# Kernel tuning notes

Measured on AMD Instinct MI355X. Metric: run time of the kernel, lower is better.

The kernel has to match this reference:

```python
import jax, jax.numpy as jnp
import numpy as np

D_MODEL = 1024
NUM_HEADS = 16
HEAD_DIM = D_MODEL // NUM_HEADS


def setup_inputs() -> dict:
    key = jax.random.key(0)
    ks = jax.random.split(key, 12)
    B, S = 2, 2048
    scale = 1.0 / np.sqrt(D_MODEL)
    inp = {
        "x": jax.random.normal(ks[0], (B, S, D_MODEL), dtype=jnp.float32),
        "docking_scores": jax.random.uniform(ks[1], (B, S), dtype=jnp.float32),
        "q_w": jax.random.normal(ks[2], (D_MODEL, D_MODEL), dtype=jnp.float32) * scale,
        "q_b": jnp.zeros((D_MODEL,), dtype=jnp.float32),
        "k_w": jax.random.normal(ks[3], (D_MODEL, D_MODEL), dtype=jnp.float32) * scale,
        "k_b": jnp.zeros((D_MODEL,), dtype=jnp.float32),
        "v_w": jax.random.normal(ks[4], (D_MODEL, D_MODEL), dtype=jnp.float32) * scale,
        "v_b": jnp.zeros((D_MODEL,), dtype=jnp.float32),
        "o_w": jax.random.normal(ks[5], (D_MODEL, D_MODEL), dtype=jnp.float32) * scale,
        "o_b": jnp.zeros((D_MODEL,), dtype=jnp.float32),
        "alpha": jnp.float32(0.5),
    }
    return inp


def reference(x, docking_scores, q_w, q_b, k_w, k_b, v_w, v_b, o_w, o_b, alpha):
    B, S, _ = x.shape
    # Projections; weights stored as (in, out) so y = x @ W + b
    def proj(w, b):
        y = jnp.einsum('bsd,de->bse', x, w) + b
        return y.reshape(B, S, NUM_HEADS, HEAD_DIM).transpose(0, 2, 1, 3)  # (B,H,S,hd)
    Q = proj(q_w, q_b)
    K = proj(k_w, k_b)
    V = proj(v_w, v_b)
    scores = jnp.einsum('bhqd,bhkd->bhqk', Q, K) / np.sqrt(HEAD_DIM)
    attn = jax.nn.softmax(scores, axis=-1)  # (B,H,S,S)
    # post-softmax docking blend, broadcast over heads and query positions
    ds = docking_scores[:, None, None, :]  # (B,1,1,S)
    attn = (1.0 - alpha) * attn + alpha * ds
    ctx = jnp.einsum('bhqk,bhkd->bhqd', attn, V)
    ctx = ctx.transpose(0, 2, 1, 3).reshape(B, S, D_MODEL)
    return jnp.einsum('bsd,de->bse', ctx, o_w) + o_b
```

## Files before the change

kernel.cpp:

```cpp
#include <hip/hip_runtime.h>
#include <hip/hip_bf16.h>

typedef __attribute__((ext_vector_type(8)))  short bf16x8;
typedef __attribute__((ext_vector_type(4)))  float f32x4;
typedef __attribute__((ext_vector_type(16))) float f32x16;
typedef __attribute__((ext_vector_type(4)))  int   i32x4;
typedef __attribute__((ext_vector_type(4)))  unsigned short u16x4;
typedef __attribute__((ext_vector_type(8)))  unsigned short u16x8;

__device__ __forceinline__ unsigned short f2bf(float f) {
    unsigned int u = __builtin_bit_cast(unsigned int, f);
    u += 0x7FFFu + ((u >> 16) & 1u);
    return (unsigned short)(u >> 16);
}
__device__ __forceinline__ float bf2f(unsigned short h) {
    unsigned int u = ((unsigned int)h) << 16;
    return __builtin_bit_cast(float, u);
}
__device__ __forceinline__ bf16x8 ld16(const unsigned short* p) {
    return *reinterpret_cast<const bf16x8*>(p);
}
__device__ __forceinline__ float fexp2(float x) {
    float r; asm("v_exp_f32 %0, %1" : "=v"(r) : "v"(x)); return r;
}
__device__ __forceinline__ float frcp(float x) {
    float r; asm("v_rcp_f32 %0, %1" : "=v"(r) : "v"(x)); return r;
}
__device__ __forceinline__ void pswap(unsigned int& a, unsigned int& b) {
    asm("v_permlane32_swap_b32 %0, %1" : "+v"(a), "+v"(b));
}

__global__ void cvt_x_kernel(const float* __restrict__ in, unsigned short* __restrict__ out, int n8) {
    int idx = blockIdx.x * blockDim.x + threadIdx.x;
    int stride = gridDim.x * blockDim.x;
    for (int i = idx; i < n8; i += stride) {
        f32x4 a = reinterpret_cast<const f32x4*>(in)[i*2];
        f32x4 b = reinterpret_cast<const f32x4*>(in)[i*2+1];
        u16x8 o;
        o[0]=f2bf(a[0]); o[1]=f2bf(a[1]); o[2]=f2bf(a[2]); o[3]=f2bf(a[3]);
        o[4]=f2bf(b[0]); o[5]=f2bf(b[1]); o[6]=f2bf(b[2]); o[7]=f2bf(b[3]);
        reinterpret_cast<u16x8*>(out)[i] = o;
    }
}

__global__ void tr_w_kernel(const float* __restrict__ q_w, const float* __restrict__ k_w,
                            const float* __restrict__ v_w, const float* __restrict__ o_w,
                            unsigned short* __restrict__ WT) {
    __shared__ float tile[32][33];
    const float* W = (blockIdx.z == 0) ? q_w : (blockIdx.z == 1) ? k_w : (blockIdx.z == 2) ? v_w : o_w;
    unsigned short* dst = WT + (size_t)blockIdx.z * 1024 * 1024;
    int tx = threadIdx.x, ty = threadIdx.y;
    int n0 = blockIdx.x * 32, k0 = blockIdx.y * 32;
#pragma unroll
    for (int j = 0; j < 4; ++j)
        tile[ty + j*8][tx] = W[(size_t)(k0 + ty + j*8) * 1024 + n0 + tx];
    __syncthreads();
#pragma unroll
    for (int j = 0; j < 4; ++j)
        dst[(size_t)(n0 + ty + j*8) * 1024 + k0 + tx] = f2bf(tile[tx][ty + j*8]);
}

__global__ __launch_bounds__(256) void gemm_qkv(
    const unsigned short* __restrict__ A,
    const unsigned short* __restrict__ WT,
    const float* __restrict__ qb, const float* __restrict__ kbias, const float* __restrict__ vbias,
    unsigned short* __restrict__ Qo, unsigned short* __restrict__ Ko, unsigned short* __restrict__ Vto)
{
    __shared__ __align__(16) unsigned short As[128*64];
    __shared__ __align__(16) unsigned short Bs[128*64];
    const int tid = threadIdx.x, lane = tid & 63, w = tid >> 6;
    const int wm = w >> 1, wn = w & 1;
    const int m0 = blockIdx.y * 128, n0 = blockIdx.x * 128;
    const int K = 1024;
    f32x4 acc[4][4] = {};
    for (int k0 = 0; k0 < K; k0 += 64) {
#pragma unroll
        for (int j = 0; j < 4; ++j) {
            const int c = j*256 + tid, r = c >> 3, s = c & 7;
            __builtin_amdgcn_global_load_lds(
                (const __attribute__((address_space(1))) void*)&A[(size_t)(m0+r)*K + k0 + s*8],
                (__attribute__((address_space(3))) void*)&As[(size_t)c*8], 16, 0, 0);
            __builtin_amdgcn_global_load_lds(
                (const __attribute__((address_space(1))) void*)&WT[(size_t)(n0+r)*K + k0 + s*8],
                (__attribute__((address_space(3))) void*)&Bs[(size_t)c*8], 16, 0, 0);
        }
        __syncthreads();
#pragma unroll
        for (int kc = 0; kc < 2; ++kc) {
            bf16x8 af[4], bfr[4];
            const int slog = kc*4 + (lane >> 4);
#pragma unroll
            for (int t = 0; t < 4; ++t) {
                const int row = wm*64 + t*16 + (lane & 15);
                af[t]  = ld16(&As[row*64 + slog*8]);
                const int col = wn*64 + t*16 + (lane & 15);
                bfr[t] = ld16(&Bs[col*64 + slog*8]);
            }
#pragma unroll
            for (int mt = 0; mt < 4; ++mt)
#pragma unroll
                for (int nt = 0; nt < 4; ++nt)
                    acc[mt][nt] = __builtin_amdgcn_mfma_f32_16x16x32_bf16(af[mt], bfr[nt], acc[mt][nt], 0, 0, 0);
        }
        __syncthreads();
    }
    const int mat = n0 >> 10;
    if (mat == 2) {
#pragma unroll
        for (int mt = 0; mt < 4; ++mt)
#pragma unroll
        for (int nt = 0; nt < 4; ++nt) {
            const int nl = (n0 & 1023) + wn*64 + nt*16 + (lane & 15);
            const int h = nl >> 6, hd = nl & 63;
            const int mbase = m0 + wm*64 + mt*16 + ((lane >> 4) << 2);
            const int b = mbase >> 11, s = mbase & 2047;
            const float bv = vbias[nl];
            u16x4 pk;
#pragma unroll
            for (int r = 0; r < 4; ++r) pk[r] = f2bf(acc[mt][nt][r] + bv);
            *reinterpret_cast<u16x4*>(&Vto[((size_t)((b << 4) | h) * 64 + hd) * 2048 + s]) = pk;
        }
    } else {
        unsigned short* outp = mat ? Ko : Qo;
        const float* bias = mat ? kbias : qb;
        const float scale = mat ? 1.0f : 0.180336881f;
#pragma unroll
        for (int mt = 0; mt < 4; ++mt)
#pragma unroll
        for (int nt = 0; nt < 4; ++nt) {
            const int nl = (n0 & 1023) + wn*64 + nt*16 + (lane & 15);
            const int h = nl >> 6, hd = nl & 63;
            const int mbase = m0 + wm*64 + mt*16 + ((lane >> 4) << 2);
            const float bv = bias[nl];
#pragma unroll
            for (int r = 0; r < 4; ++r) {
                const int mm2 = mbase + r, b = mm2 >> 11, s = mm2 & 2047;
                outp[((size_t)((b << 4) | h) * 2048 + s) * 64 + hd] = f2bf((acc[mt][nt][r] + bv) * scale);
            }
        }
    }
}

__global__ __launch_bounds__(256) void gemm_o(
    const unsigned short* __restrict__ A, const unsigned short* __restrict__ WT,
    const float* __restrict__ bias, float* __restrict__ Cout)
{
    __shared__ __align__(16) unsigned short As[128*64];
    __shared__ __align__(16) unsigned short Bs[128*64];
    const int tid = threadIdx.x, lane = tid & 63, w = tid >> 6;
    const int wm = w >> 1, wn = w & 1;
    const int m0 = blockIdx.y * 128, n0 = blockIdx.x * 128;
    const int K = 1024;
    f32x4 acc[4][4] = {};
    for (int k0 = 0; k0 < K; k0 += 64) {
#pragma unroll
        for (int j = 0; j < 4; ++j) {
            const int c = j*256 + tid, r = c >> 3, s = c & 7;
            __builtin_amdgcn_global_load_lds(
                (const __attribute__((address_space(1))) void*)&A[(size_t)(m0+r)*K + k0 + s*8],
                (__attribute__((address_space(3))) void*)&As[(size_t)c*8], 16, 0, 0);
            __builtin_amdgcn_global_load_lds(
                (const __attribute__((address_space(1))) void*)&WT[(size_t)(n0+r)*K + k0 + s*8],
                (__attribute__((address_space(3))) void*)&Bs[(size_t)c*8], 16, 0, 0);
        }
        __syncthreads();
#pragma unroll
        for (int kc = 0; kc < 2; ++kc) {
            bf16x8 af[4], bfr[4];
            const int slog = kc*4 + (lane >> 4);
#pragma unroll
            for (int t = 0; t < 4; ++t) {
                const int row = wm*64 + t*16 + (lane & 15);
                af[t]  = ld16(&As[row*64 + slog*8]);
                const int col = wn*64 + t*16 + (lane & 15);
                bfr[t] = ld16(&Bs[col*64 + slog*8]);
            }
#pragma unroll
            for (int mt = 0; mt < 4; ++mt)
#pragma unroll
                for (int nt = 0; nt < 4; ++nt)
                    acc[mt][nt] = __builtin_amdgcn_mfma_f32_16x16x32_bf16(af[mt], bfr[nt], acc[mt][nt], 0, 0, 0);
        }
        __syncthreads();
    }
#pragma unroll
    for (int mt = 0; mt < 4; ++mt)
#pragma unroll
    for (int nt = 0; nt < 4; ++nt) {
        const int n = n0 + wn*64 + nt*16 + (lane & 15);
        const int mbase = m0 + wm*64 + mt*16 + ((lane >> 4) << 2);
        const float bv = bias[n];
#pragma unroll
        for (int r = 0; r < 4; ++r)
            Cout[(size_t)(mbase + r) * 1024 + n] = acc[mt][nt][r] + bv;
    }
}

__global__ void dock_c_kernel(const float* __restrict__ ds, const unsigned short* __restrict__ Vt,
                              float* __restrict__ cvec) {
    __shared__ float red[256];
    const int bh = blockIdx.x >> 3, sl = blockIdx.x & 7;
    const int b = bh >> 4;
    const int t = threadIdx.x, d = t & 63, q4 = t >> 6;
    const unsigned short* vrow = &Vt[(size_t)bh * 131072 + (size_t)d * 2048 + sl * 256 + q4 * 64];
    const float* dsr = &ds[b * 2048 + sl * 256 + q4 * 64];
    float sum = 0.f;
#pragma unroll
    for (int k = 0; k < 64; k += 8) {
        bf16x8 v = ld16(&vrow[k]);
#pragma unroll
        for (int i = 0; i < 8; ++i) sum += dsr[k + i] * bf2f((unsigned short)v[i]);
    }
    red[t] = sum;
    __syncthreads();
    if (t < 64) atomicAdd(&cvec[bh * 64 + t], red[t] + red[64 + t] + red[128 + t] + red[192 + t]);
}

__global__ __launch_bounds__(256, 2) void attn_kernel(
    const unsigned short* __restrict__ Qp,
    const unsigned short* __restrict__ Kp,
    const unsigned short* __restrict__ Vp,
    const float* __restrict__ cvec,
    const float* __restrict__ alpha_p,
    unsigned short* __restrict__ ctx)
{
    __shared__ __align__(16) unsigned short Ks[2][4096];
    __shared__ __align__(16) unsigned short Vs[2][4096];
    __shared__ float sml[4][32];
    const int tid = threadIdx.x, lane = tid & 63, w = tid >> 6;
    const int hi = lane >> 5, ln = lane & 31;
    const int wg = blockIdx.x;
    const int swz = (wg & 7) * 64 + (wg >> 3);
    const int bh = swz >> 4, qt = swz & 15;
    const int q0 = qt * 128 + w * 32;
    const size_t hb = (size_t)bh * (2048 * 64);
    const float alpha = *alpha_p;

    const int sr = tid >> 3, ss = tid & 7;
    const int ssw = (ss ^ (sr & 7)) << 3;
    const unsigned short* Kg = Kp + hb;
    const unsigned short* Vg = Vp + hb;

    bf16x8 qf[4];
    {
        const unsigned short* qr = &Qp[hb + (size_t)(q0 + ln) * 64 + hi * 8];
#pragma unroll
        for (int ks = 0; ks < 4; ++ks) qf[ks] = ld16(qr + ks * 16);
    }

    const short one_bf = (short)0x3F80;
    const bf16x8 onesf = {one_bf, one_bf, one_bf, one_bf, one_bf, one_bf, one_bf, one_bf};

    f32x16 oacc0 = {}, oacc1 = {}, lacc = {};
    float m = -1e30f;

    auto stage = [&](int buf, int it) {
#pragma unroll
        for (int p = 0; p < 2; ++p) {
            __builtin_amdgcn_global_load_lds(
                (const __attribute__((address_space(1))) void*)&Kg[(size_t)(it*64 + p*32 + sr) * 64 + ssw],
                (__attribute__((address_space(3))) void*)&Ks[buf][p*2048 + tid*8], 16, 0, 0);
            __builtin_amdgcn_global_load_lds(
                (const __attribute__((address_space(1))) void*)&Vg[(size_t)(p*32 + sr) * 2048 + it*64 + ssw],
                (__attribute__((address_space(3))) void*)&Vs[buf][p*2048 + tid*8], 16, 0, 0);
        }
    };

    bf16x8 kf[8];
    auto ldk = [&](const unsigned short* base) {
#pragma unroll
        for (int t2 = 0; t2 < 2; ++t2)
#pragma unroll
        for (int ks = 0; ks < 4; ++ks) {
            const int row = t2*32 + ln;
            const int sl  = ((ks*2 + hi) ^ (row & 7)) << 3;
            kf[t2*4+ks] = ld16(base + row*64 + sl);
        }
    };

    stage(0, 0);
    __syncthreads();
    stage(1, 1);
    ldk(&Ks[0][0]);
    f32x16 sA0 = {}, sA1 = {}, sB0 = {}, sB1 = {};
#pragma unroll
    for (int ks = 0; ks < 4; ++ks) {
        sA0 = __builtin_amdgcn_mfma_f32_32x32x16_bf16(kf[ks],   qf[ks], sA0, 0, 0, 0);
        sA1 = __builtin_amdgcn_mfma_f32_32x32x16_bf16(kf[4+ks], qf[ks], sA1, 0, 0, 0);
    }

    auto step = [&](f32x16& sc0, f32x16& sc1, f32x16& sn0, f32x16& sn1, int buf, int it) {
        bf16x8 vf[8];
#pragma unroll
        for (int t2 = 0; t2 < 2; ++t2)
#pragma unroll
        for (int ks = 0; ks < 4; ++ks) {
            const int row = t2*32 + ln;
            const int sl  = ((ks*2 + hi) ^ (row & 7)) << 3;
            vf[t2*4+ks] = ld16(&Vs[buf][row*64 + sl]);
        }
        __syncthreads();
        if (it + 2 < 32) stage(buf, it + 2);
        const bool more = (it + 1 < 32);
        if (more) ldk(&Ks[buf ^ 1][0]);
        __builtin_amdgcn_s_setprio(1);
        if (more) {
            sn0 = {}; sn1 = {};
#pragma unroll
            for (int ks = 0; ks < 4; ++ks) {
                sn0 = __builtin_amdgcn_mfma_f32_32x32x16_bf16(kf[ks],   qf[ks], sn0, 0, 0, 0);
                sn1 = __builtin_amdgcn_mfma_f32_32x32x16_bf16(kf[4+ks], qf[ks], sn1, 0, 0, 0);
            }
        }
        float mx[8];
#pragma unroll
        for (int r = 0; r < 8; ++r)
            mx[r] = fmaxf(fmaxf(sc0[r], sc0[r+8]), fmaxf(sc1[r], sc1[r+8]));
        float tm = fmaxf(fmaxf(fmaxf(mx[0],mx[1]), fmaxf(mx[2],mx[3])),
                         fmaxf(fmaxf(mx[4],mx[5]), fmaxf(mx[6],mx[7])));
        {
            unsigned int ua = __builtin_bit_cast(unsigned int, tm), ub = ua;
            pswap(ua, ub);
            tm = fmaxf(__builtin_bit_cast(float, ua), __builtin_bit_cast(float, ub));
        }
        if (__any(tm > m + 8.f)) {
            float mn = fmaxf(m, tm);
            float sc = fexp2(m - mn);
            m = mn;
            if (hi == 0) sml[w][ln] = sc;
#pragma unroll
            for (int m4 = 0; m4 < 4; ++m4) {
                f32x4 sv = *reinterpret_cast<const f32x4*>(&sml[w][m4*8 + hi*4]);
#pragma unroll
                for (int r3 = 0; r3 < 4; ++r3) {
                    oacc0[m4*4+r3] *= sv[r3];
                    oacc1[m4*4+r3] *= sv[r3];
                    lacc [m4*4+r3] *= sv[r3];
                }
            }
        }
        float p0a[16], p1a[16];
#pragma unroll
        for (int r = 0; r < 16; ++r) {
            p0a[r] = fexp2(sc0[r] - m);
            p1a[r] = fexp2(sc1[r] - m);
        }

        unsigned int Wp0[4][2], Wp1[4][2];
#pragma unroll
        for (int m4 = 0; m4 < 4; ++m4)
#pragma unroll
        for (int jj = 0; jj < 2; ++jj) {
            asm("v_cvt_pk_bf16_f32 %0, %1, %2" : "=v"(Wp0[m4][jj]) : "v"(p0a[m4*4+jj*2]), "v"(p0a[m4*4+jj*2+1]));
            asm("v_cvt_pk_bf16_f32 %0, %1, %2" : "=v"(Wp1[m4][jj]) : "v"(p1a[m4*4+jj*2]), "v"(p1a[m4*4+jj*2+1]));
        }
#pragma unroll
        for (int ks = 0; ks < 4; ++ks) {
            const int tp = ks & 1;
            unsigned int a0, a1, b0, b1;
            if (ks < 2) { a0 = Wp0[2*tp][0]; a1 = Wp0[2*tp][1]; b0 = Wp0[2*tp+1][0]; b1 = Wp0[2*tp+1][1]; }
            else        { a0 = Wp1[2*tp][0]; a1 = Wp1[2*tp][1]; b0 = Wp1[2*tp+1][0]; b1 = Wp1[2*tp+1][1]; }
            pswap(a0, b0);
            pswap(a1, b1);
            i32x4 pw;
            pw[0] = (int)a0; pw[1] = (int)a1; pw[2] = (int)b0; pw[3] = (int)b1;
            bf16x8 pf = __builtin_bit_cast(bf16x8, pw);
            oacc0 = __builtin_amdgcn_mfma_f32_32x32x16_bf16(pf, vf[ks],   oacc0, 0, 0, 0);
            oacc1 = __builtin_amdgcn_mfma_f32_32x32x16_bf16(pf, vf[4+ks], oacc1, 0, 0, 0);
            lacc  = __builtin_amdgcn_mfma_f32_32x32x16_bf16(pf, onesf,    lacc,  0, 0, 0);
        }
        __builtin_amdgcn_s_setprio(0);
    };

#pragma unroll 1
    for (int ii = 0; ii < 16; ++ii) {
        step(sA0, sA1, sB0, sB1, 0, ii*2);
        step(sB0, sB1, sA0, sA1, 1, ii*2 + 1);
    }

    const int b = bh >> 4, h = bh & 15;
    const float a1f = 1.f - alpha;
    const float cv0 = alpha * cvec[bh*64 + ln];
    const float cv1 = alpha * cvec[bh*64 + 32 + ln];
#pragma unroll
    for (int m4 = 0; m4 < 4; ++m4) {
#pragma unroll
        for (int r3 = 0; r3 < 4; ++r3) {
            const int row = m4*8 + hi*4 + r3;
            const int s = q0 + row;
            const float iv = frcp(lacc[m4*4 + r3]);
            unsigned short* orow = &ctx[((size_t)(b*2048 + s))*1024 + h*64 + ln];
            orow[0]  = f2bf(a1f * oacc0[m4*4+r3] * iv + cv0);
            orow[32] = f2bf(a1f * oacc1[m4*4+r3] * iv + cv1);
        }
    }
}

extern "C" void kernel_launch(void* const* d_in, const int* in_sizes, int n_in,
                              void* d_out, int out_size, void* d_ws, size_t ws_size,
                              hipStream_t stream) {
    const float* x     = (const float*)d_in[0];
    const float* ds    = (const float*)d_in[1];
    const float* q_w   = (const float*)d_in[2];
    const float* q_b   = (const float*)d_in[3];
    const float* k_w   = (const float*)d_in[4];
    const float* k_b   = (const float*)d_in[5];
    const float* v_w   = (const float*)d_in[6];
    const float* v_b   = (const float*)d_in[7];
    const float* o_w   = (const float*)d_in[8];
    const float* o_b   = (const float*)d_in[9];
    const float* alpha = (const float*)d_in[10];

    char* ws = (char*)d_ws;
    const size_t MB = 1024 * 1024;
    unsigned short* xb   = (unsigned short*)(ws);
    unsigned short* wT   = (unsigned short*)(ws + 8  * MB);
    unsigned short* Qb   = (unsigned short*)(ws + 16 * MB);
    unsigned short* Kb   = (unsigned short*)(ws + 24 * MB);
    unsigned short* Vt   = (unsigned short*)(ws + 32 * MB);
    float*          cvec = (float*)         (ws + 40 * MB);
    unsigned short* ctxb = xb;

    const int M = 4096, K = 1024;

    cvt_x_kernel<<<2048, 256, 0, stream>>>(x, xb, M * K / 8);

    dim3 tb(32, 8);
    dim3 tg(32, 32, 4);
    tr_w_kernel<<<tg, tb, 0, stream>>>(q_w, k_w, v_w, o_w, wT);

    dim3 gqkv(24, 32);
    gemm_qkv<<<gqkv, 256, 0, stream>>>(xb, wT, q_b, k_b, v_b, Qb, Kb, Vt);

    hipMemsetAsync(cvec, 0, 32 * 64 * sizeof(float), stream);
    dock_c_kernel<<<256, 256, 0, stream>>>(ds, Vt, cvec);

    attn_kernel<<<512, 256, 0, stream>>>(Qb, Kb, Vt, cvec, alpha, ctxb);

    dim3 go(8, 32);
    gemm_o<<<go, 256, 0, stream>>>(ctxb, wT + (size_t)3 * MB, o_b, (float*)d_out);
}
```

Baseline: 144.9 us.

## Double-buffer LDS and XOR-swizzle tiles in QKV and output projection GEMMs

Both projection GEMMs now use two LDS buffers, so the next K tile is prefetched with global_load_lds while MFMAs run on the current one, and one barrier per iteration is dropped. The source column chunk is XOR-swizzled by row so the later 16-byte LDS fragment reads avoid bank conflicts. LDS use per block doubles to 64KB, which may lower occupancy. The single barrier now guards both buffers, so the next stage is issued only after all waves have finished reading the previous buffer.

```diff
diff --git a/kernel.cpp b/kernel.cpp
--- a/kernel.cpp
+++ b/kernel.cpp
@@ -66,35 +66,46 @@
     const float* __restrict__ qb, const float* __restrict__ kbias, const float* __restrict__ vbias,
     unsigned short* __restrict__ Qo, unsigned short* __restrict__ Ko, unsigned short* __restrict__ Vto)
 {
-    __shared__ __align__(16) unsigned short As[128*64];
-    __shared__ __align__(16) unsigned short Bs[128*64];
+    __shared__ __align__(16) unsigned short As[2][128*64];
+    __shared__ __align__(16) unsigned short Bs[2][128*64];
     const int tid = threadIdx.x, lane = tid & 63, w = tid >> 6;
     const int wm = w >> 1, wn = w & 1;
     const int m0 = blockIdx.y * 128, n0 = blockIdx.x * 128;
     const int K = 1024;
+    const int sr = tid >> 3, ssl = tid & 7;
+    const int ssw = (ssl ^ (sr & 7)) << 3;
     f32x4 acc[4][4] = {};
-    for (int k0 = 0; k0 < K; k0 += 64) {
+
+    auto stage = [&](int buf, int k0) {
 #pragma unroll
         for (int j = 0; j < 4; ++j) {
-            const int c = j*256 + tid, r = c >> 3, s = c & 7;
-            __builtin_amdgcn_global_load_lds(
-                (const __attribute__((address_space(1))) void*)&A[(size_t)(m0+r)*K + k0 + s*8],
-                (__attribute__((address_space(3))) void*)&As[(size_t)c*8], 16, 0, 0);
-            __builtin_amdgcn_global_load_lds(
-                (const __attribute__((address_space(1))) void*)&WT[(size_t)(n0+r)*K + k0 + s*8],
-                (__attribute__((address_space(3))) void*)&Bs[(size_t)c*8], 16, 0, 0);
-        }
+            const int c = j*256 + tid, r = j*32 + sr;
+            __builtin_amdgcn_global_load_lds(
+                (const __attribute__((address_space(1))) void*)&A[(size_t)(m0+r)*K + k0 + ssw],
+                (__attribute__((address_space(3))) void*)&As[buf][(size_t)c*8], 16, 0, 0);
+            __builtin_amdgcn_global_load_lds(
+                (const __attribute__((address_space(1))) void*)&WT[(size_t)(n0+r)*K + k0 + ssw],
+                (__attribute__((address_space(3))) void*)&Bs[buf][(size_t)c*8], 16, 0, 0);
+        }
+    };
+
+    stage(0, 0);
+#pragma unroll 1
+    for (int t = 0; t < 16; ++t) {
         __syncthreads();
+        if (t < 15) stage((t + 1) & 1, (t + 1) * 64);
+        const unsigned short* pa = &As[t & 1][0];
+        const unsigned short* pb = &Bs[t & 1][0];
 #pragma unroll
         for (int kc = 0; kc < 2; ++kc) {
             bf16x8 af[4], bfr[4];
             const int slog = kc*4 + (lane >> 4);
 #pragma unroll
-            for (int t = 0; t < 4; ++t) {
-                const int row = wm*64 + t*16 + (lane & 15);
-                af[t]  = ld16(&As[row*64 + slog*8]);
-                const int col = wn*64 + t*16 + (lane & 15);
-                bfr[t] = ld16(&Bs[col*64 + slog*8]);
+            for (int t2 = 0; t2 < 4; ++t2) {
+                const int row = wm*64 + t2*16 + (lane & 15);
+                af[t2]  = ld16(&pa[row*64 + ((slog ^ (row & 7)) << 3)]);
+                const int col = wn*64 + t2*16 + (lane & 15);
+                bfr[t2] = ld16(&pb[col*64 + ((slog ^ (col & 7)) << 3)]);
             }
 #pragma unroll
             for (int mt = 0; mt < 4; ++mt)
@@ -102,7 +113,6 @@
                 for (int nt = 0; nt < 4; ++nt)
                     acc[mt][nt] = __builtin_amdgcn_mfma_f32_16x16x32_bf16(af[mt], bfr[nt], acc[mt][nt], 0, 0, 0);
         }
-        __syncthreads();
     }
     const int mat = n0 >> 10;
     if (mat == 2) {
@@ -145,35 +155,46 @@
     const unsigned short* __restrict__ A, const unsigned short* __restrict__ WT,
     const float* __restrict__ bias, float* __restrict__ Cout)
 {
-    __shared__ __align__(16) unsigned short As[128*64];
-    __shared__ __align__(16) unsigned short Bs[128*64];
+    __shared__ __align__(16) unsigned short As[2][128*64];
+    __shared__ __align__(16) unsigned short Bs[2][128*64];
     const int tid = threadIdx.x, lane = tid & 63, w = tid >> 6;
     const int wm = w >> 1, wn = w & 1;
     const int m0 = blockIdx.y * 128, n0 = blockIdx.x * 128;
     const int K = 1024;
+    const int sr = tid >> 3, ssl = tid & 7;
+    const int ssw = (ssl ^ (sr & 7)) << 3;
     f32x4 acc[4][4] = {};
-    for (int k0 = 0; k0 < K; k0 += 64) {
+
+    auto stage = [&](int buf, int k0) {
 #pragma unroll
         for (int j = 0; j < 4; ++j) {
-            const int c = j*256 + tid, r = c >> 3, s = c & 7;
-            __builtin_amdgcn_global_load_lds(
-                (const __attribute__((address_space(1))) void*)&A[(size_t)(m0+r)*K + k0 + s*8],
-                (__attribute__((address_space(3))) void*)&As[(size_t)c*8], 16, 0, 0);
-            __builtin_amdgcn_global_load_lds(
-                (const __attribute__((address_space(1))) void*)&WT[(size_t)(n0+r)*K + k0 + s*8],
-                (__attribute__((address_space(3))) void*)&Bs[(size_t)c*8], 16, 0, 0);
-        }
+            const int c = j*256 + tid, r = j*32 + sr;
+            __builtin_amdgcn_global_load_lds(
+                (const __attribute__((address_space(1))) void*)&A[(size_t)(m0+r)*K + k0 + ssw],
+                (__attribute__((address_space(3))) void*)&As[buf][(size_t)c*8], 16, 0, 0);
+            __builtin_amdgcn_global_load_lds(
+                (const __attribute__((address_space(1))) void*)&WT[(size_t)(n0+r)*K + k0 + ssw],
+                (__attribute__((address_space(3))) void*)&Bs[buf][(size_t)c*8], 16, 0, 0);
+        }
+    };
+
+    stage(0, 0);
+#pragma unroll 1
+    for (int t = 0; t < 16; ++t) {
         __syncthreads();
+        if (t < 15) stage((t + 1) & 1, (t + 1) * 64);
+        const unsigned short* pa = &As[t & 1][0];
+        const unsigned short* pb = &Bs[t & 1][0];
 #pragma unroll
         for (int kc = 0; kc < 2; ++kc) {
             bf16x8 af[4], bfr[4];
             const int slog = kc*4 + (lane >> 4);
 #pragma unroll
-            for (int t = 0; t < 4; ++t) {
-                const int row = wm*64 + t*16 + (lane & 15);
-                af[t]  = ld16(&As[row*64 + slog*8]);
-                const int col = wn*64 + t*16 + (lane & 15);
-                bfr[t] = ld16(&Bs[col*64 + slog*8]);
+            for (int t2 = 0; t2 < 4; ++t2) {
+                const int row = wm*64 + t2*16 + (lane & 15);
+                af[t2]  = ld16(&pa[row*64 + ((slog ^ (row & 7)) << 3)]);
+                const int col = wn*64 + t2*16 + (lane & 15);
+                bfr[t2] = ld16(&pb[col*64 + ((slog ^ (col & 7)) << 3)]);
             }
 #pragma unroll
             for (int mt = 0; mt < 4; ++mt)
@@ -181,7 +202,6 @@
                 for (int nt = 0; nt < 4; ++nt)
                     acc[mt][nt] = __builtin_amdgcn_mfma_f32_16x16x32_bf16(af[mt], bfr[nt], acc[mt][nt], 0, 0, 0);
         }
-        __syncthreads();
     }
 #pragma unroll
     for (int mt = 0; mt < 4; ++mt)
```

After: 127.7 us. -11.8%, faster.
